# Performance work log

Hardware: AMD Instinct MI355X
Metric: run time of the kernel (lower is better)

## Reference

```python
import jax, jax.numpy as jnp
import numpy as np

B, C, H, W = 8, 64, 128, 128
OC, KH, KW = 64, 3, 3
STRIDE, PAD, DIL = 1, 1, 1
DG = 1            # deformable groups
G = 1             # conv groups
K = KH * KW
HO = (H + 2 * PAD - DIL * (KH - 1) - 1) // STRIDE + 1
WO = (W + 2 * PAD - DIL * (KW - 1) - 1) // STRIDE + 1


def setup_inputs() -> dict:
    key = jax.random.key(0)
    k1, k2, k3, k4 = jax.random.split(key, 4)
    input_tensor = jax.random.normal(k1, (B, C, H, W), dtype=jnp.float32)
    offset = jax.random.normal(k2, (B, DG * 2 * K, HO, WO), dtype=jnp.float32)
    mask = jax.random.uniform(k3, (B, DG * K, HO, WO), dtype=jnp.float32)
    n = C * KH * KW
    std_v = 1.0 / np.sqrt(n)
    weight = jax.random.uniform(k4, (OC, C // G, KH, KW), dtype=jnp.float32,
                                minval=-std_v, maxval=std_v)
    bias = jnp.zeros((OC,), dtype=jnp.float32)
    return {"input_tensor": input_tensor, "offset": offset, "mask": mask,
            "weight": weight, "bias": bias}


def _bilinear_sample(img, py, px):
    # img: [Cg, H, W]; py, px: [K, HO, WO] fractional sample coords
    y0 = jnp.floor(py).astype(jnp.int32)
    x0 = jnp.floor(px).astype(jnp.int32)
    y1, x1 = y0 + 1, x0 + 1
    wy1 = py - y0.astype(py.dtype)
    wx1 = px - x0.astype(px.dtype)
    wy0, wx0 = 1.0 - wy1, 1.0 - wx1

    def gather(yy, xx):
        valid = ((yy >= 0) & (yy < H) & (xx >= 0) & (xx < W)).astype(img.dtype)
        yc = jnp.clip(yy, 0, H - 1)
        xc = jnp.clip(xx, 0, W - 1)
        return img[:, yc, xc] * valid  # [Cg, K, HO, WO], zero outside

    return (gather(y0, x0) * (wy0 * wx0) + gather(y0, x1) * (wy0 * wx1)
            + gather(y1, x0) * (wy1 * wx0) + gather(y1, x1) * (wy1 * wx1))


def _mdconv(input_tensor, offset, mask, weight, bias):
    Cg = C // DG
    ky = (jnp.arange(K) // KW).astype(jnp.float32)   # kernel row per tap
    kx = (jnp.arange(K) % KW).astype(jnp.float32)    # kernel col per tap
    oy = jnp.arange(HO, dtype=jnp.float32) * STRIDE - PAD
    ox = jnp.arange(WO, dtype=jnp.float32) * STRIDE - PAD
    base_y = ky[:, None] * DIL + oy[None, :]         # [K, HO]
    base_x = kx[:, None] * DIL + ox[None, :]         # [K, WO]

    off = offset.reshape(B, DG, K, 2, HO, WO)
    py = base_y[None, None, :, :, None] + off[:, :, :, 0]  # [B, DG, K, HO, WO]
    px = base_x[None, None, :, None, :] + off[:, :, :, 1]

    imgs = input_tensor.reshape(B, DG, Cg, H, W)
    sample = jax.vmap(jax.vmap(_bilinear_sample))           # over B then DG
    cols = sample(imgs, py, px)                             # [B, DG, Cg, K, HO, WO]
    cols = cols * mask.reshape(B, DG, 1, K, HO, WO)
    cols = cols.reshape(B, G, C // G, K, HO, WO)

    w = weight.reshape(G, OC // G, C // G, K)
    out = jnp.einsum('gock,bgckpq->bgopq', w, cols)
    out = out.reshape(B, OC, HO, WO) + bias[None, :, None, None]
    return out


def reference(input_tensor, offset, mask, weight, bias):
    return _mdconv(input_tensor, offset, mask, weight, bias)
```

## Files before the change

kernel.cpp:

```cpp
#include <hip/hip_runtime.h>
#include <stdint.h>

typedef unsigned short u16;

#define B_ 8
#define C_ 64
#define H_ 128
#define W_ 128
#define OC_ 64
#define HO_ 128
#define WO_ 128
#define HWC_ (H_*W_*C_)
#define PADW 72

typedef __attribute__((ext_vector_type(8))) _Float16 f16x8;
typedef __attribute__((ext_vector_type(2))) _Float16 h2;
typedef __attribute__((ext_vector_type(4))) float f32x4;

__device__ __forceinline__ u16 f2h(float f) {
  union { _Float16 h; u16 u; } c; c.h = (_Float16)f; return c.u;
}
__device__ __forceinline__ uint32_t pkh2(float f) {
  union { _Float16 h[2]; uint32_t u; } c;
  const _Float16 h = (_Float16)f;
  c.h[0] = h; c.h[1] = h; return c.u;
}

__global__ void wprep_kernel(const float* __restrict__ w, u16* __restrict__ wk2) {
  const int idx = blockIdx.x * 256 + threadIdx.x;
  const int j    = idx & 7;
  const int lane = (idx >> 3) & 63;
  const int kk   = (idx >> 9) & 1;
  const int m    = (idx >> 10) & 1;
  const int wr   = (idx >> 11) & 1;
  const int k    = idx >> 12;
  const int oc = wr*32 + m*16 + (lane & 15);
  const int c  = kk*32 + (lane >> 4)*8 + j;
  wk2[idx] = f2h(w[(oc*C_ + c)*9 + k]);
}

__global__ __launch_bounds__(256) void nhwc_kernel(const float* __restrict__ in,
                                                   u16* __restrict__ nhwc) {
  __shared__ float t[64][65];
  const int b = blockIdx.z, h = blockIdx.y, w0 = blockIdx.x * 64;
  const int tid = threadIdx.x;
  for (int idx = tid; idx < 64*64; idx += 256) {
    int c = idx >> 6, w = idx & 63;
    t[w][c] = in[((b*C_ + c)*H_ + h)*W_ + w0 + w];
  }
  __syncthreads();
  for (int idx = tid; idx < 64*64; idx += 256) {
    int w = idx >> 6, c = idx & 63;
    nhwc[((b*H_ + h)*W_ + w0 + w)*C_ + c] = f2h(t[w][c]);
  }
}

__device__ __forceinline__ uint32_t blendh(uint32_t g00, uint32_t g01,
                                           uint32_t g10, uint32_t g11, uint4 w) {
  h2 s = __builtin_bit_cast(h2, g00) * __builtin_bit_cast(h2, w.x)
       + __builtin_bit_cast(h2, g01) * __builtin_bit_cast(h2, w.y)
       + __builtin_bit_cast(h2, g10) * __builtin_bit_cast(h2, w.z)
       + __builtin_bit_cast(h2, g11) * __builtin_bit_cast(h2, w.w);
  return __builtin_bit_cast(uint32_t, s);
}

__global__ __launch_bounds__(256, 4) void mdconv_main(
    const float* __restrict__ offs, const float* __restrict__ mask,
    const float* __restrict__ bias, const u16* __restrict__ nhwc,
    const u16* __restrict__ wk2, float* __restrict__ out)
{
  __shared__ u16 clds[64*PADW];
  __shared__ int2 pA[576];
  __shared__ uint4 pW[576];

  const int tid = threadIdx.x;
  const int lane = tid & 63;
  const int wv = tid >> 6;
  const int b = blockIdx.z;
  const int p = blockIdx.y;
  const int q0 = blockIdx.x * 64;

  for (int item = tid; item < 576; item += 256) {
    const int k = item >> 6;
    const int px = item & 63;
    const int q = q0 + px;
    const int ky = k / 3, kx = k % 3;
    const float oy = offs[((b*18 + 2*k)*HO_ + p)*WO_ + q];
    const float ox = offs[((b*18 + 2*k + 1)*HO_ + p)*WO_ + q];
    const float mm = mask[((b*9 + k)*HO_ + p)*WO_ + q];
    const float py  = (float)(ky + p - 1) + oy;
    const float pxx = (float)(kx + q - 1) + ox;
    const float y0f = floorf(py), x0f = floorf(pxx);
    const int y0 = (int)y0f, x0 = (int)x0f;
    const int y1 = y0 + 1, x1 = x0 + 1;
    const float wy1 = py - y0f, wx1 = pxx - x0f;
    const float wy0 = 1.f - wy1, wx0 = 1.f - wx1;
    const bool vy0 = (y0 >= 0) & (y0 < H_);
    const bool vy1 = (y1 >= 0) & (y1 < H_);
    const bool vx0 = (x0 >= 0) & (x0 < W_);
    const bool vx1 = (x1 >= 0) & (x1 < W_);
    const float w00 = (vy0 & vx0) ? wy0*wx0*mm : 0.f;
    const float w01 = (vy0 & vx1) ? wy0*wx1*mm : 0.f;
    const float w10 = (vy1 & vx0) ? wy1*wx0*mm : 0.f;
    const float w11 = (vy1 & vx1) ? wy1*wx1*mm : 0.f;
    const int y0c = min(max(y0,0),H_-1), y1c = min(max(y1,0),H_-1);
    const int x0c = min(max(x0,0),W_-1), x1c = min(max(x1,0),W_-1);
    const int dx = (x1c - x0c) * C_;
    const int dy = (y1c - y0c) * W_ * C_;
    pA[item] = make_int2(b*HWC_ + (y0c*W_ + x0c)*C_, dx | (dy << 16));
    pW[item] = make_uint4(pkh2(w00), pkh2(w01), pkh2(w10), pkh2(w11));
  }
  __syncthreads();

  f32x4 acc00 = {0.f,0.f,0.f,0.f};
  f32x4 acc01 = acc00, acc10 = acc00, acc11 = acc00;
  const int wr = wv >> 1, wc = wv & 1;
  const int px0 = tid >> 3;
  const int c8 = (tid & 7) * 8;

  for (int k = 0; k < 9; ++k) {
    const u16* wg = wk2 + (k*2 + wr)*2048 + lane*8;
    const f16x8 a00 = *(const f16x8*)(wg);
    const f16x8 a01 = *(const f16x8*)(wg + 512);
    const f16x8 a10 = *(const f16x8*)(wg + 1024);
    const f16x8 a11 = *(const f16x8*)(wg + 1536);

    {
      const int piA = k*64 + px0, piB = piA + 32;
      const int2 aA = pA[piA];
      const int2 aB = pA[piB];
      const uint4 wA = pW[piA];
      const uint4 wB = pW[piB];
      const u16* sA = nhwc + aA.x + c8;
      const u16* sB = nhwc + aB.x + c8;
      const int dxA = aA.y & 0xFFFF, dyA = ((uint32_t)aA.y) >> 16;
      const int dxB = aB.y & 0xFFFF, dyB = ((uint32_t)aB.y) >> 16;
      const uint4 gA00 = *(const uint4*)(sA);
      const uint4 gA01 = *(const uint4*)(sA + dxA);
      const uint4 gA10 = *(const uint4*)(sA + dyA);
      const uint4 gA11 = *(const uint4*)(sA + dyA + dxA);
      const uint4 gB00 = *(const uint4*)(sB);
      const uint4 gB01 = *(const uint4*)(sB + dxB);
      const uint4 gB10 = *(const uint4*)(sB + dyB);
      const uint4 gB11 = *(const uint4*)(sB + dyB + dxB);
      uint4 rA, rB;
      rA.x = blendh(gA00.x, gA01.x, gA10.x, gA11.x, wA);
      rA.y = blendh(gA00.y, gA01.y, gA10.y, gA11.y, wA);
      rA.z = blendh(gA00.z, gA01.z, gA10.z, gA11.z, wA);
      rA.w = blendh(gA00.w, gA01.w, gA10.w, gA11.w, wA);
      rB.x = blendh(gB00.x, gB01.x, gB10.x, gB11.x, wB);
      rB.y = blendh(gB00.y, gB01.y, gB10.y, gB11.y, wB);
      rB.z = blendh(gB00.z, gB01.z, gB10.z, gB11.z, wB);
      rB.w = blendh(gB00.w, gB01.w, gB10.w, gB11.w, wB);
      *(uint4*)(&clds[px0*PADW + c8]) = rA;
      *(uint4*)(&clds[(px0+32)*PADW + c8]) = rB;
    }
    __syncthreads();

    const f16x8 b00 = *(const f16x8*)(&clds[(wc*32 + (lane & 15))*PADW + (lane >> 4)*8]);
    const f16x8 b01 = *(const f16x8*)(&clds[(wc*32 + (lane & 15))*PADW + (lane >> 4)*8 + 32]);
    const f16x8 b10 = *(const f16x8*)(&clds[(wc*32 + 16 + (lane & 15))*PADW + (lane >> 4)*8]);
    const f16x8 b11 = *(const f16x8*)(&clds[(wc*32 + 16 + (lane & 15))*PADW + (lane >> 4)*8 + 32]);
    acc00 = __builtin_amdgcn_mfma_f32_16x16x32_f16(a00, b00, acc00, 0, 0, 0);
    acc00 = __builtin_amdgcn_mfma_f32_16x16x32_f16(a01, b01, acc00, 0, 0, 0);
    acc01 = __builtin_amdgcn_mfma_f32_16x16x32_f16(a00, b10, acc01, 0, 0, 0);
    acc01 = __builtin_amdgcn_mfma_f32_16x16x32_f16(a01, b11, acc01, 0, 0, 0);
    acc10 = __builtin_amdgcn_mfma_f32_16x16x32_f16(a10, b00, acc10, 0, 0, 0);
    acc10 = __builtin_amdgcn_mfma_f32_16x16x32_f16(a11, b01, acc10, 0, 0, 0);
    acc11 = __builtin_amdgcn_mfma_f32_16x16x32_f16(a10, b10, acc11, 0, 0, 0);
    acc11 = __builtin_amdgcn_mfma_f32_16x16x32_f16(a11, b11, acc11, 0, 0, 0);
    if (k < 8) __syncthreads();
  }

  const int qc = q0 + wc*32 + (lane & 15);
  const int ocr = wr*32 + (lane >> 4)*4;
  #pragma unroll
  for (int m = 0; m < 2; ++m) {
    #pragma unroll
    for (int n = 0; n < 2; ++n) {
      const f32x4 a = (m==0) ? (n==0 ? acc00 : acc01) : (n==0 ? acc10 : acc11);
      #pragma unroll
      for (int j = 0; j < 4; ++j) {
        const int oc = ocr + m*16 + j;
        out[((b*OC_ + oc)*HO_ + p)*WO_ + qc + n*16] = a[j] + bias[oc];
      }
    }
  }
}

extern "C" void kernel_launch(void* const* d_in, const int* in_sizes, int n_in,
                              void* d_out, int out_size, void* d_ws, size_t ws_size,
                              hipStream_t stream) {
  const float* input  = (const float*)d_in[0];
  const float* offset = (const float*)d_in[1];
  const float* mask   = (const float*)d_in[2];
  const float* weight = (const float*)d_in[3];
  const float* bias   = (const float*)d_in[4];
  float* out = (float*)d_out;

  u16* nhwc = (u16*)d_ws;
  u16* wk2  = nhwc + (size_t)B_*H_*W_*C_;

  hipLaunchKernelGGL(wprep_kernel, dim3(144), dim3(256), 0, stream, weight, wk2);
  hipLaunchKernelGGL(nhwc_kernel, dim3(2, 128, 8), dim3(256), 0, stream, input, nhwc);
  hipLaunchKernelGGL(mdconv_main, dim3(2, 128, 8), dim3(256), 0, stream,
                     offset, mask, bias, nhwc, wk2, out);
}
```

Before: 57.53 us.

## Software-pipeline bilinear gathers two taps ahead with double-buffered LDS

Restructures the 9-tap loop so global gathers for tap k+2 and weight loads for tap k+1 are issued before the MFMAs of tap k. The gathered column tile is blended into a double-buffered LDS slot, which allows one barrier per tap instead of two. A custom barrier waits only on LDS counters, so outstanding global loads stay in flight across it. The extra register buffers lower the occupancy target from 4 to 3 blocks per CU, which trades latency hiding through more waves for latency hiding through prefetch.

```diff
diff --git a/kernel.cpp b/kernel.cpp
--- a/kernel.cpp
+++ b/kernel.cpp
@@ -64,12 +64,18 @@
   return __builtin_bit_cast(uint32_t, s);
 }
 
-__global__ __launch_bounds__(256, 4) void mdconv_main(
+#define RBAR() { \
+    asm volatile("s_waitcnt lgkmcnt(0)" ::: "memory"); \
+    __builtin_amdgcn_sched_barrier(0); \
+    __builtin_amdgcn_s_barrier(); \
+    __builtin_amdgcn_sched_barrier(0); }
+
+__global__ __launch_bounds__(256, 3) void mdconv_main(
     const float* __restrict__ offs, const float* __restrict__ mask,
     const float* __restrict__ bias, const u16* __restrict__ nhwc,
     const u16* __restrict__ wk2, float* __restrict__ out)
 {
-  __shared__ u16 clds[64*PADW];
+  __shared__ u16 clds[2][64*PADW];
   __shared__ int2 pA[576];
   __shared__ uint4 pW[576];
 
@@ -118,59 +124,74 @@
   const int px0 = tid >> 3;
   const int c8 = (tid & 7) * 8;
 
-  for (int k = 0; k < 9; ++k) {
-    const u16* wg = wk2 + (k*2 + wr)*2048 + lane*8;
-    const f16x8 a00 = *(const f16x8*)(wg);
-    const f16x8 a01 = *(const f16x8*)(wg + 512);
-    const f16x8 a10 = *(const f16x8*)(wg + 1024);
-    const f16x8 a11 = *(const f16x8*)(wg + 1536);
-
-    {
-      const int piA = k*64 + px0, piB = piA + 32;
-      const int2 aA = pA[piA];
-      const int2 aB = pA[piB];
-      const uint4 wA = pW[piA];
-      const uint4 wB = pW[piB];
-      const u16* sA = nhwc + aA.x + c8;
-      const u16* sB = nhwc + aB.x + c8;
-      const int dxA = aA.y & 0xFFFF, dyA = ((uint32_t)aA.y) >> 16;
-      const int dxB = aB.y & 0xFFFF, dyB = ((uint32_t)aB.y) >> 16;
-      const uint4 gA00 = *(const uint4*)(sA);
-      const uint4 gA01 = *(const uint4*)(sA + dxA);
-      const uint4 gA10 = *(const uint4*)(sA + dyA);
-      const uint4 gA11 = *(const uint4*)(sA + dyA + dxA);
-      const uint4 gB00 = *(const uint4*)(sB);
-      const uint4 gB01 = *(const uint4*)(sB + dxB);
-      const uint4 gB10 = *(const uint4*)(sB + dyB);
-      const uint4 gB11 = *(const uint4*)(sB + dyB + dxB);
-      uint4 rA, rB;
-      rA.x = blendh(gA00.x, gA01.x, gA10.x, gA11.x, wA);
-      rA.y = blendh(gA00.y, gA01.y, gA10.y, gA11.y, wA);
-      rA.z = blendh(gA00.z, gA01.z, gA10.z, gA11.z, wA);
-      rA.w = blendh(gA00.w, gA01.w, gA10.w, gA11.w, wA);
-      rB.x = blendh(gB00.x, gB01.x, gB10.x, gB11.x, wB);
-      rB.y = blendh(gB00.y, gB01.y, gB10.y, gB11.y, wB);
-      rB.z = blendh(gB00.z, gB01.z, gB10.z, gB11.z, wB);
-      rB.w = blendh(gB00.w, gB01.w, gB10.w, gB11.w, wB);
-      *(uint4*)(&clds[px0*PADW + c8]) = rA;
-      *(uint4*)(&clds[(px0+32)*PADW + c8]) = rB;
-    }
-    __syncthreads();
-
-    const f16x8 b00 = *(const f16x8*)(&clds[(wc*32 + (lane & 15))*PADW + (lane >> 4)*8]);
-    const f16x8 b01 = *(const f16x8*)(&clds[(wc*32 + (lane & 15))*PADW + (lane >> 4)*8 + 32]);
-    const f16x8 b10 = *(const f16x8*)(&clds[(wc*32 + 16 + (lane & 15))*PADW + (lane >> 4)*8]);
-    const f16x8 b11 = *(const f16x8*)(&clds[(wc*32 + 16 + (lane & 15))*PADW + (lane >> 4)*8 + 32]);
-    acc00 = __builtin_amdgcn_mfma_f32_16x16x32_f16(a00, b00, acc00, 0, 0, 0);
-    acc00 = __builtin_amdgcn_mfma_f32_16x16x32_f16(a01, b01, acc00, 0, 0, 0);
-    acc01 = __builtin_amdgcn_mfma_f32_16x16x32_f16(a00, b10, acc01, 0, 0, 0);
-    acc01 = __builtin_amdgcn_mfma_f32_16x16x32_f16(a01, b11, acc01, 0, 0, 0);
-    acc10 = __builtin_amdgcn_mfma_f32_16x16x32_f16(a10, b00, acc10, 0, 0, 0);
-    acc10 = __builtin_amdgcn_mfma_f32_16x16x32_f16(a11, b01, acc10, 0, 0, 0);
-    acc11 = __builtin_amdgcn_mfma_f32_16x16x32_f16(a10, b10, acc11, 0, 0, 0);
-    acc11 = __builtin_amdgcn_mfma_f32_16x16x32_f16(a11, b11, acc11, 0, 0, 0);
-    if (k < 8) __syncthreads();
-  }
+  uint4 g0[8], g1[8];
+  f16x8 a0[4], a1[4];
+
+#define ISSUE_G(kk_, gbuf) { \
+    const int piA = (kk_)*64 + px0, piB = piA + 32; \
+    const int2 aA = pA[piA]; const int2 aB = pA[piB]; \
+    const u16* sA = nhwc + aA.x + c8; \
+    const u16* sB = nhwc + aB.x + c8; \
+    const int dxA = aA.y & 0xFFFF, dyA = ((uint32_t)aA.y) >> 16; \
+    const int dxB = aB.y & 0xFFFF, dyB = ((uint32_t)aB.y) >> 16; \
+    gbuf[0] = *(const uint4*)(sA);       gbuf[1] = *(const uint4*)(sA + dxA); \
+    gbuf[2] = *(const uint4*)(sA + dyA); gbuf[3] = *(const uint4*)(sA + dyA + dxA); \
+    gbuf[4] = *(const uint4*)(sB);       gbuf[5] = *(const uint4*)(sB + dxB); \
+    gbuf[6] = *(const uint4*)(sB + dyB); gbuf[7] = *(const uint4*)(sB + dyB + dxB); }
+
+#define LOADA(kk_, areg) { \
+    const u16* wg = wk2 + ((kk_)*2 + wr)*2048 + lane*8; \
+    areg[0] = *(const f16x8*)(wg);        areg[1] = *(const f16x8*)(wg + 512); \
+    areg[2] = *(const f16x8*)(wg + 1024); areg[3] = *(const f16x8*)(wg + 1536); }
+
+#define BLEND_WR(kk_, gbuf) { \
+    const int piA = (kk_)*64 + px0, piB = piA + 32; \
+    const uint4 wA = pW[piA]; const uint4 wB = pW[piB]; \
+    uint4 rA, rB; \
+    rA.x = blendh(gbuf[0].x, gbuf[1].x, gbuf[2].x, gbuf[3].x, wA); \
+    rA.y = blendh(gbuf[0].y, gbuf[1].y, gbuf[2].y, gbuf[3].y, wA); \
+    rA.z = blendh(gbuf[0].z, gbuf[1].z, gbuf[2].z, gbuf[3].z, wA); \
+    rA.w = blendh(gbuf[0].w, gbuf[1].w, gbuf[2].w, gbuf[3].w, wA); \
+    rB.x = blendh(gbuf[4].x, gbuf[5].x, gbuf[6].x, gbuf[7].x, wB); \
+    rB.y = blendh(gbuf[4].y, gbuf[5].y, gbuf[6].y, gbuf[7].y, wB); \
+    rB.z = blendh(gbuf[4].z, gbuf[5].z, gbuf[6].z, gbuf[7].z, wB); \
+    rB.w = blendh(gbuf[4].w, gbuf[5].w, gbuf[6].w, gbuf[7].w, wB); \
+    *(uint4*)(&clds[(kk_)&1][px0*PADW + c8]) = rA; \
+    *(uint4*)(&clds[(kk_)&1][(px0+32)*PADW + c8]) = rB; }
+
+#define REGION(k_, GCUR, GNXT, ACUR, ANXT) { \
+    const u16* cb = &clds[(k_)&1][(wc*32 + (lane & 15))*PADW + (lane >> 4)*8]; \
+    const f16x8 b00 = *(const f16x8*)(cb); \
+    const f16x8 b01 = *(const f16x8*)(cb + 32); \
+    const f16x8 b10 = *(const f16x8*)(cb + 16*PADW); \
+    const f16x8 b11 = *(const f16x8*)(cb + 16*PADW + 32); \
+    if ((k_) + 2 <= 8) ISSUE_G((k_)+2, GCUR); \
+    if ((k_) + 1 <= 8) LOADA((k_)+1, ANXT); \
+    acc00 = __builtin_amdgcn_mfma_f32_16x16x32_f16(ACUR[0], b00, acc00, 0, 0, 0); \
+    acc00 = __builtin_amdgcn_mfma_f32_16x16x32_f16(ACUR[1], b01, acc00, 0, 0, 0); \
+    acc01 = __builtin_amdgcn_mfma_f32_16x16x32_f16(ACUR[0], b10, acc01, 0, 0, 0); \
+    acc01 = __builtin_amdgcn_mfma_f32_16x16x32_f16(ACUR[1], b11, acc01, 0, 0, 0); \
+    acc10 = __builtin_amdgcn_mfma_f32_16x16x32_f16(ACUR[2], b00, acc10, 0, 0, 0); \
+    acc10 = __builtin_amdgcn_mfma_f32_16x16x32_f16(ACUR[3], b01, acc10, 0, 0, 0); \
+    acc11 = __builtin_amdgcn_mfma_f32_16x16x32_f16(ACUR[2], b10, acc11, 0, 0, 0); \
+    acc11 = __builtin_amdgcn_mfma_f32_16x16x32_f16(ACUR[3], b11, acc11, 0, 0, 0); \
+    if ((k_) + 1 <= 8) { BLEND_WR((k_)+1, GNXT); RBAR(); } }
+
+  ISSUE_G(0, g0);
+  ISSUE_G(1, g1);
+  LOADA(0, a0);
+  BLEND_WR(0, g0);
+  RBAR();
+
+  REGION(0, g0, g1, a0, a1);
+  REGION(1, g1, g0, a1, a0);
+  REGION(2, g0, g1, a0, a1);
+  REGION(3, g1, g0, a1, a0);
+  REGION(4, g0, g1, a0, a1);
+  REGION(5, g1, g0, a1, a0);
+  REGION(6, g0, g1, a0, a1);
+  REGION(7, g1, g0, a1, a0);
+  REGION(8, g0, g1, a0, a1);
 
   const int qc = q0 + wc*32 + (lane & 15);
   const int ocr = wr*32 + (lane >> 4)*4;
```

After: 55.87 us. 2.9% less time.
